# Kernel optimization log

Hardware: AMD Instinct MI355X
Metric: run time of the kernel (lower is better)

The kernel has to match this reference:

```python
import jax, jax.numpy as jnp
import numpy as np

N = 50000
E = 600000
D_IN = 128
D_HID = 128


def gcn_conv(x, src, dst, ew, W, b):
    """PyG-style GCNConv with self-loops and symmetric normalization.
    x: [N, Fin], src/dst: [E'], ew: [E'], W: [Fin, Fout], b: [Fout].
    """
    n = x.shape[0]
    # degree from incoming edge weights (self-loops already appended)
    deg = jax.ops.segment_sum(ew, dst, num_segments=n)
    dinv = jnp.where(deg > 0, jax.lax.rsqrt(deg), 0.0)
    norm = dinv[src] * ew * dinv[dst]  # [E']
    h = x @ W  # linear transform first (PyG order)
    msg = h[src] * norm[:, None]  # gather + scale, [E', Fout]
    out = jax.ops.segment_sum(msg, dst, num_segments=n)  # scatter-add
    return out + b


def setup_inputs() -> dict:
    key = jax.random.key(0)
    k1, k2, k3, k4, k5, k6, k7 = jax.random.split(key, 7)
    x = jax.random.normal(k1, (N, D_IN), dtype=jnp.float32)
    edge_index = jax.random.randint(k2, (2, E), 0, N, dtype=jnp.int64)
    edge_weight = jax.random.uniform(k3, (E,), dtype=jnp.float32)
    s1 = 1.0 / np.sqrt(D_IN)
    s2 = 1.0 / np.sqrt(D_HID)
    W1 = jax.random.uniform(k4, (D_IN, D_HID), dtype=jnp.float32, minval=-s1, maxval=s1)
    b1 = jax.random.uniform(k5, (D_HID,), dtype=jnp.float32, minval=-s1, maxval=s1)
    W2 = jax.random.uniform(k6, (D_HID, D_IN), dtype=jnp.float32, minval=-s2, maxval=s2)
    b2 = jax.random.uniform(k7, (D_IN,), dtype=jnp.float32, minval=-s2, maxval=s2)
    return {"x": x, "edge_index": edge_index, "edge_weight": edge_weight,
            "W1": W1, "b1": b1, "W2": W2, "b2": b2}


def reference(x, edge_index, edge_weight, W1, b1, W2, b2):
    n = x.shape[0]
    loops = jnp.arange(n, dtype=edge_index.dtype)
    src = jnp.concatenate([edge_index[0], loops])
    dst = jnp.concatenate([edge_index[1], loops])
    ew = jnp.concatenate([edge_weight, jnp.ones((n,), dtype=edge_weight.dtype)])
    h = gcn_conv(x, src, dst, ew, W1, b1)
    h = jax.nn.relu(h)
    h = gcn_conv(h, src, dst, ew, W2, b2)
    return jax.nn.sigmoid(h)
```

## Files before the change

### kernel.cpp

```cpp
#include <hip/hip_runtime.h>
#include <math.h>


typedef unsigned int uint32;
typedef unsigned long long u64;
typedef __attribute__((ext_vector_type(8))) short bf16x8;
typedef __attribute__((ext_vector_type(4))) float f32x4;

__device__ __forceinline__ unsigned short f2bf(float f) {
    uint32 b = __float_as_uint(f);
    return (unsigned short)((b + 0x7FFFu + ((b >> 16) & 1u)) >> 16);
}

__device__ __forceinline__ float2 bf2_decode(uint32 u) {
    return make_float2(__uint_as_float(u << 16),
                       __uint_as_float(u & 0xFFFF0000u));
}

__global__ __launch_bounds__(256) void k_hist(const int* __restrict__ dst,
                                              const float* __restrict__ ew,
                                              u64* __restrict__ packed,
                                              int* __restrict__ rank, int e, int nNodes,
                                              const float* __restrict__ W1,
                                              const float* __restrict__ W2,
                                              unsigned short* __restrict__ WT1,
                                              unsigned short* __restrict__ WT2,
                                              int nbE) {
    const int b = blockIdx.x;
    if (b >= nbE) {
        int j = (b - nbE) * 256 + threadIdx.x;
        int k = j >> 7, nn = j & 127;
        WT1[nn * 128 + k] = f2bf(W1[k * 128 + nn]);
        WT2[nn * 128 + k] = f2bf(W2[k * 128 + nn]);
        return;
    }
    int i = b * 256 + threadIdx.x;
    if (i < e) {
        int d = dst[i];
        int r = b & 7;
        u64 add = (1ULL << 44) + (u64)(ew[i] * 4294967296.0f);
        u64 old = atomicAdd(&packed[(size_t)r * nNodes + d], add);
        rank[i] = (int)(old >> 44);
    }
}

__global__ __launch_bounds__(256) void k_scan1(const u64* __restrict__ packed,
                                               float* __restrict__ dinv,
                                               u64* __restrict__ bases,
                                               int* __restrict__ out,
                                               int* __restrict__ sums, int nNodes) {
    __shared__ int s[256];
    const int t = threadIdx.x;
    const int base = blockIdx.x * 1024 + t * 4;
    const int n = nNodes + 1;
    int v[4];
    #pragma unroll
    for (int u = 0; u < 4; ++u) {
        int idx = base + u;
        int c = 0;
        if (idx < nNodes) {
            const u64 mask = (1ULL << 44) - 1;
            u64 ssum = 0;
            u64 bs = 0;
            uint32 cum = 0;
            #pragma unroll
            for (int r = 0; r < 8; ++r) {
                u64 pv = packed[(size_t)r * nNodes + idx];
                bs |= (u64)cum << (8 * r);
                cum += (uint32)(pv >> 44);
                ssum += (pv & mask);
            }
            c = (int)cum;
            float deg = 1.0f + (float)ssum * (1.0f / 4294967296.0f);
            dinv[idx] = rsqrtf(deg);
            bases[idx] = bs;
        }
        v[u] = c;
    }
    s[t] = v[0] + v[1] + v[2] + v[3];
    __syncthreads();
    #pragma unroll
    for (int off = 1; off < 256; off <<= 1) {
        int x = (t >= off) ? s[t - off] : 0;
        __syncthreads();
        s[t] += x;
        __syncthreads();
    }
    if (t == 255) sums[blockIdx.x] = s[255];
    int e = (t == 0) ? 0 : s[t - 1];
    if (base + 0 < n) out[base + 0] = e;
    if (base + 1 < n) out[base + 1] = e + v[0];
    if (base + 2 < n) out[base + 2] = e + v[0] + v[1];
    if (base + 3 < n) out[base + 3] = e + v[0] + v[1] + v[2];
}

__global__ __launch_bounds__(256) void k_scan2(int* __restrict__ sums, int g) {
    __shared__ int s[256];
    const int t = threadIdx.x;
    s[t] = (t < g) ? sums[t] : 0;
    __syncthreads();
    #pragma unroll
    for (int off = 1; off < 256; off <<= 1) {
        int x = (t >= off) ? s[t - off] : 0;
        __syncthreads();
        s[t] += x;
        __syncthreads();
    }
    if (t < g) sums[t] = (t == 0) ? 0 : s[t - 1];
}

__global__ __launch_bounds__(256) void k_fill(const int* __restrict__ src,
                                              const int* __restrict__ dst,
                                              const float* __restrict__ ew,
                                              const float* __restrict__ dinv,
                                              const int* __restrict__ rowptr,
                                              const int* __restrict__ csums,
                                              const u64* __restrict__ bases,
                                              const int* __restrict__ rank,
                                              float2* __restrict__ csr, int e) {
    int i = blockIdx.x * 256 + threadIdx.x;
    if (i < e) {
        int s = src[i], d = dst[i];
        int r = blockIdx.x & 7;
        float nrm = dinv[s] * ew[i] * dinv[d];
        int pos = rowptr[d] + csums[d >> 10]
                + (int)((bases[d] >> (8 * r)) & 0xFF) + rank[i];
        csr[pos] = make_float2(__int_as_float(s), nrm);
    }
}

template <int AFP32>
__global__ __launch_bounds__(256) void k_gemm(const void* __restrict__ Ap,
                                              const unsigned short* __restrict__ WT,
                                              unsigned short* __restrict__ H, int n) {
    const int lane = threadIdx.x & 63;
    const int wv   = threadIdx.x >> 6;
    const int quad = lane >> 4;
    const int l16  = lane & 15;
    const int m0   = blockIdx.x * 128 + wv * 32;
    f32x4 acc[2][8] = {};

    #pragma unroll
    for (int ks = 0; ks < 4; ++ks) {
        const int k0 = ks * 32 + quad * 8;
        bf16x8 a[2];
        #pragma unroll
        for (int rt = 0; rt < 2; ++rt) {
            int row = m0 + rt * 16 + l16;
            if (row >= n) row = n - 1;
            if (AFP32) {
                const float* Af = (const float*)Ap + (size_t)row * 128 + k0;
                float4 f0 = *(const float4*)(Af);
                float4 f1 = *(const float4*)(Af + 4);
                bf16x8 v;
                v[0] = (short)f2bf(f0.x); v[1] = (short)f2bf(f0.y);
                v[2] = (short)f2bf(f0.z); v[3] = (short)f2bf(f0.w);
                v[4] = (short)f2bf(f1.x); v[5] = (short)f2bf(f1.y);
                v[6] = (short)f2bf(f1.z); v[7] = (short)f2bf(f1.w);
                a[rt] = v;
            } else {
                const unsigned short* Ab = (const unsigned short*)Ap + (size_t)row * 128 + k0;
                a[rt] = *(const bf16x8*)Ab;
            }
        }
        #pragma unroll
        for (int ct = 0; ct < 8; ++ct) {
            bf16x8 b = *(const bf16x8*)(WT + (size_t)(ct * 16 + l16) * 128 + k0);
            acc[0][ct] = __builtin_amdgcn_mfma_f32_16x16x32_bf16(a[0], b, acc[0][ct], 0, 0, 0);
            acc[1][ct] = __builtin_amdgcn_mfma_f32_16x16x32_bf16(a[1], b, acc[1][ct], 0, 0, 0);
        }
    }

    #pragma unroll
    for (int rt = 0; rt < 2; ++rt) {
        #pragma unroll
        for (int r = 0; r < 4; ++r) {
            int row = m0 + rt * 16 + quad * 4 + r;
            if (row < n) {
                unsigned short* o = H + (size_t)row * 128 + l16;
                #pragma unroll
                for (int ct = 0; ct < 8; ++ct)
                    o[ct * 16] = f2bf(acc[rt][ct][r]);
            }
        }
    }
}

__device__ __forceinline__ void fma8(float* acc, uint4 u, float w) {
    float2 f;
    f = bf2_decode(u.x); acc[0] += f.x * w; acc[1] += f.y * w;
    f = bf2_decode(u.y); acc[2] += f.x * w; acc[3] += f.y * w;
    f = bf2_decode(u.z); acc[4] += f.x * w; acc[5] += f.y * w;
    f = bf2_decode(u.w); acc[6] += f.x * w; acc[7] += f.y * w;
}

template <int ACT>
__global__ __launch_bounds__(256) void k_gather(const uint4* __restrict__ Hb4,
                                                const float2* __restrict__ csr,
                                                const int* __restrict__ rowptr,
                                                const int* __restrict__ csums,
                                                const float* __restrict__ dinv,
                                                const float4* __restrict__ bias4,
                                                void* __restrict__ outp, int N) {
    int node = blockIdx.x * 4 + (threadIdx.x >> 6);
    if (node >= N) return;
    const int lane = threadIdx.x & 63;
    const int q = lane >> 4, l = lane & 15;
    const int start = rowptr[node] + csums[node >> 10];
    const int end   = rowptr[node + 1] + csums[(node + 1) >> 10];

    float di = dinv[node];
    float selfw = (q == 0) ? di * di : 0.0f;
    float acc[8] = {};
    fma8(acc, Hb4[(size_t)node * 16 + l], selfw);

    for (int k = start; k < end; k += 16) {
        float2 c[4];
        float w[4];
        uint4 u[4];
        #pragma unroll
        for (int j = 0; j < 4; ++j) {
            int ej = k + q + 4 * j;
            c[j] = csr[ej < end ? ej : end - 1];
            w[j] = (ej < end) ? c[j].y : 0.0f;
        }
        #pragma unroll
        for (int j = 0; j < 4; ++j)
            u[j] = Hb4[(size_t)__float_as_int(c[j].x) * 16 + l];
        #pragma unroll
        for (int j = 0; j < 4; ++j)
            fma8(acc, u[j], w[j]);
    }

    #pragma unroll
    for (int j = 0; j < 8; ++j) {
        acc[j] += __shfl_xor(acc[j], 16, 64);
        acc[j] += __shfl_xor(acc[j], 32, 64);
    }

    if (q == 0) {
        float4 b0 = bias4[l * 2], b1 = bias4[l * 2 + 1];
        acc[0] += b0.x; acc[1] += b0.y; acc[2] += b0.z; acc[3] += b0.w;
        acc[4] += b1.x; acc[5] += b1.y; acc[6] += b1.z; acc[7] += b1.w;
        if (ACT == 0) {
            #pragma unroll
            for (int j = 0; j < 8; ++j) acc[j] = fmaxf(acc[j], 0.0f);
            uint4 o;
            o.x = (uint32)f2bf(acc[0]) | ((uint32)f2bf(acc[1]) << 16);
            o.y = (uint32)f2bf(acc[2]) | ((uint32)f2bf(acc[3]) << 16);
            o.z = (uint32)f2bf(acc[4]) | ((uint32)f2bf(acc[5]) << 16);
            o.w = (uint32)f2bf(acc[6]) | ((uint32)f2bf(acc[7]) << 16);
            ((uint4*)outp)[(size_t)node * 16 + l] = o;
        } else {
            #pragma unroll
            for (int j = 0; j < 8; ++j) acc[j] = 1.0f / (1.0f + expf(-acc[j]));
            float4* o4 = (float4*)outp + (size_t)node * 32 + l * 2;
            o4[0] = make_float4(acc[0], acc[1], acc[2], acc[3]);
            o4[1] = make_float4(acc[4], acc[5], acc[6], acc[7]);
        }
    }
}

extern "C" void kernel_launch(void* const* d_in, const int* in_sizes, int n_in,
                              void* d_out, int out_size, void* d_ws, size_t ws_size,
                              hipStream_t stream) {
    const float* x  = (const float*)d_in[0];
    const int*   ei = (const int*)d_in[1];
    const float* ew = (const float*)d_in[2];
    const float* W1 = (const float*)d_in[3];
    const float* b1 = (const float*)d_in[4];
    const float* W2 = (const float*)d_in[5];
    const float* b2 = (const float*)d_in[6];

    const int N = in_sizes[0] / 128;
    const int E = in_sizes[2];
    const int* src = ei;
    const int* dst = ei + E;
    float* out = (float*)d_out;

    auto align = [](size_t v) { return (v + 255) & ~(size_t)255; };
    char* p = (char*)d_ws;
    float*  dinv   = (float*)p;   p += align((size_t)N * 4);
    int*    rowptr = (int*)p;     p += align((size_t)(N + 1) * 4);
    int*    csums  = (int*)p;     p += align((size_t)1024 * 4);
    u64*    bases  = (u64*)p;     p += align((size_t)N * 8);
    unsigned short* WT1 = (unsigned short*)p; p += align((size_t)128 * 128 * 2);
    unsigned short* WT2 = (unsigned short*)p; p += align((size_t)128 * 128 * 2);
    int*    rank   = (int*)p;     p += align((size_t)E * 4);
    float2* csr    = (float2*)p;  p += align((size_t)E * 8);
    unsigned short* h  = (unsigned short*)p; p += align((size_t)N * 128 * 2);
    unsigned short* g1 = (unsigned short*)p;
    u64* packed = (u64*)g1;

    const int nbE = (E + 255) / 256;
    const int gScan = (N + 1 + 1023) / 1024;
    const int gGemm = (N + 127) / 128;
    const int gGath = (N + 3) / 4;

    hipMemsetAsync(packed, 0, (size_t)8 * N * 8, stream);
    k_hist<<<nbE + 64, 256, 0, stream>>>(dst, ew, packed, rank, E, N,
                                         W1, W2, WT1, WT2, nbE);
    k_scan1<<<gScan, 256, 0, stream>>>(packed, dinv, bases, rowptr, csums, N);
    k_scan2<<<1, 256, 0, stream>>>(csums, gScan);
    k_fill<<<nbE, 256, 0, stream>>>(src, dst, ew, dinv, rowptr, csums, bases,
                                    rank, csr, E);

    k_gemm<1><<<gGemm, 256, 0, stream>>>(x, WT1, h, N);
    k_gather<0><<<gGath, 256, 0, stream>>>((const uint4*)h, csr, rowptr, csums,
                                           dinv, (const float4*)b1, g1, N);

    k_gemm<0><<<gGemm, 256, 0, stream>>>(g1, WT2, h, N);
    k_gather<1><<<gGath, 256, 0, stream>>>((const uint4*)h, csr, rowptr, csums,
                                           dinv, (const float4*)b2, out, N);
}
```

Before: 227.8 us.

## Fuse memset/transpose init, merge first GEMM with histogram, single-pass scan

Replaces the memset and histogram launch with an init kernel that zeroes the packed counters and transposes the weights. The first GEMM is merged into the histogram launch so MFMA blocks and atomic blocks share one grid. The two scan kernels become one, with a last-block-done atomic counter doing the block-sum scan. This removes several launches and lets independent work overlap, at the cost of acquire/release atomics and a mixed-work grid that may balance poorly.

```diff
diff --git a/kernel.cpp b/kernel.cpp
--- a/kernel.cpp
+++ b/kernel.cpp
@@ -17,39 +17,112 @@
                        __uint_as_float(u & 0xFFFF0000u));
 }
 
-__global__ __launch_bounds__(256) void k_hist(const int* __restrict__ dst,
-                                              const float* __restrict__ ew,
-                                              u64* __restrict__ packed,
-                                              int* __restrict__ rank, int e, int nNodes,
+template <int AFP32>
+__device__ __forceinline__ void gemm_body(const void* __restrict__ Ap,
+                                          const unsigned short* __restrict__ WT,
+                                          unsigned short* __restrict__ H,
+                                          int n, int tb) {
+    const int lane = threadIdx.x & 63;
+    const int wv   = threadIdx.x >> 6;
+    const int quad = lane >> 4;
+    const int l16  = lane & 15;
+    const int m0   = tb * 128 + wv * 32;
+    f32x4 acc[2][8] = {};
+
+    #pragma unroll
+    for (int ks = 0; ks < 4; ++ks) {
+        const int k0 = ks * 32 + quad * 8;
+        bf16x8 a[2];
+        #pragma unroll
+        for (int rt = 0; rt < 2; ++rt) {
+            int row = m0 + rt * 16 + l16;
+            if (row >= n) row = n - 1;
+            if (AFP32) {
+                const float* Af = (const float*)Ap + (size_t)row * 128 + k0;
+                float4 f0 = *(const float4*)(Af);
+                float4 f1 = *(const float4*)(Af + 4);
+                bf16x8 v;
+                v[0] = (short)f2bf(f0.x); v[1] = (short)f2bf(f0.y);
+                v[2] = (short)f2bf(f0.z); v[3] = (short)f2bf(f0.w);
+                v[4] = (short)f2bf(f1.x); v[5] = (short)f2bf(f1.y);
+                v[6] = (short)f2bf(f1.z); v[7] = (short)f2bf(f1.w);
+                a[rt] = v;
+            } else {
+                const unsigned short* Ab = (const unsigned short*)Ap + (size_t)row * 128 + k0;
+                a[rt] = *(const bf16x8*)Ab;
+            }
+        }
+        #pragma unroll
+        for (int ct = 0; ct < 8; ++ct) {
+            bf16x8 b = *(const bf16x8*)(WT + (size_t)(ct * 16 + l16) * 128 + k0);
+            acc[0][ct] = __builtin_amdgcn_mfma_f32_16x16x32_bf16(a[0], b, acc[0][ct], 0, 0, 0);
+            acc[1][ct] = __builtin_amdgcn_mfma_f32_16x16x32_bf16(a[1], b, acc[1][ct], 0, 0, 0);
+        }
+    }
+
+    #pragma unroll
+    for (int rt = 0; rt < 2; ++rt) {
+        #pragma unroll
+        for (int r = 0; r < 4; ++r) {
+            int row = m0 + rt * 16 + quad * 4 + r;
+            if (row < n) {
+                unsigned short* o = H + (size_t)row * 128 + l16;
+                #pragma unroll
+                for (int ct = 0; ct < 8; ++ct)
+                    o[ct * 16] = f2bf(acc[rt][ct][r]);
+            }
+        }
+    }
+}
+
+__global__ __launch_bounds__(256) void k_init(u64* __restrict__ packed, int n4,
+                                              int* __restrict__ done,
                                               const float* __restrict__ W1,
                                               const float* __restrict__ W2,
                                               unsigned short* __restrict__ WT1,
-                                              unsigned short* __restrict__ WT2,
-                                              int nbE) {
-    const int b = blockIdx.x;
-    if (b >= nbE) {
-        int j = (b - nbE) * 256 + threadIdx.x;
+                                              unsigned short* __restrict__ WT2) {
+    int idx = blockIdx.x * 256 + threadIdx.x;
+    if (idx < n4) ((uint4*)packed)[idx] = make_uint4(0u, 0u, 0u, 0u);
+    if (idx == 0) *done = 0;
+    if (blockIdx.x < 64) {
+        int j = blockIdx.x * 256 + threadIdx.x;
         int k = j >> 7, nn = j & 127;
         WT1[nn * 128 + k] = f2bf(W1[k * 128 + nn]);
         WT2[nn * 128 + k] = f2bf(W2[k * 128 + nn]);
+    }
+}
+
+__global__ __launch_bounds__(256) void k_gemm1_hist(const float* __restrict__ x,
+                                                    const unsigned short* __restrict__ WT1,
+                                                    unsigned short* __restrict__ h,
+                                                    const int* __restrict__ dst,
+                                                    const float* __restrict__ ew,
+                                                    u64* __restrict__ packed,
+                                                    int* __restrict__ rank,
+                                                    int E, int N, int gGemm) {
+    const int b = blockIdx.x;
+    if (b < gGemm) {
+        gemm_body<1>(x, WT1, h, N, b);
         return;
     }
-    int i = b * 256 + threadIdx.x;
-    if (i < e) {
+    int i = (b - gGemm) * 256 + threadIdx.x;
+    if (i < E) {
         int d = dst[i];
-        int r = b & 7;
+        int r = (i >> 8) & 7;
         u64 add = (1ULL << 44) + (u64)(ew[i] * 4294967296.0f);
-        u64 old = atomicAdd(&packed[(size_t)r * nNodes + d], add);
+        u64 old = atomicAdd(&packed[(size_t)r * N + d], add);
         rank[i] = (int)(old >> 44);
     }
 }
 
-__global__ __launch_bounds__(256) void k_scan1(const u64* __restrict__ packed,
-                                               float* __restrict__ dinv,
-                                               u64* __restrict__ bases,
-                                               int* __restrict__ out,
-                                               int* __restrict__ sums, int nNodes) {
+__global__ __launch_bounds__(256) void k_scan(const u64* __restrict__ packed,
+                                              float* __restrict__ dinv,
+                                              u64* __restrict__ bases,
+                                              int* __restrict__ rowptr,
+                                              int* __restrict__ csums,
+                                              int* __restrict__ done, int nNodes) {
     __shared__ int s[256];
+    __shared__ int lastFlag;
     const int t = threadIdx.x;
     const int base = blockIdx.x * 1024 + t * 4;
     const int n = nNodes + 1;
@@ -86,27 +159,35 @@
         s[t] += x;
         __syncthreads();
     }
-    if (t == 255) sums[blockIdx.x] = s[255];
+    if (t == 255)
+        __hip_atomic_store(&csums[blockIdx.x], s[255], __ATOMIC_RELEASE,
+                           __HIP_MEMORY_SCOPE_AGENT);
     int e = (t == 0) ? 0 : s[t - 1];
-    if (base + 0 < n) out[base + 0] = e;
-    if (base + 1 < n) out[base + 1] = e + v[0];
-    if (base + 2 < n) out[base + 2] = e + v[0] + v[1];
-    if (base + 3 < n) out[base + 3] = e + v[0] + v[1] + v[2];
-}
-
-__global__ __launch_bounds__(256) void k_scan2(int* __restrict__ sums, int g) {
-    __shared__ int s[256];
-    const int t = threadIdx.x;
-    s[t] = (t < g) ? sums[t] : 0;
+    if (base + 0 < n) rowptr[base + 0] = e;
+    if (base + 1 < n) rowptr[base + 1] = e + v[0];
+    if (base + 2 < n) rowptr[base + 2] = e + v[0] + v[1];
+    if (base + 3 < n) rowptr[base + 3] = e + v[0] + v[1] + v[2];
+
     __syncthreads();
-    #pragma unroll
-    for (int off = 1; off < 256; off <<= 1) {
-        int x = (t >= off) ? s[t - off] : 0;
-        __syncthreads();
-        s[t] += x;
-        __syncthreads();
-    }
-    if (t < g) sums[t] = (t == 0) ? 0 : s[t - 1];
+    if (t == 0) {
+        int prev = __hip_atomic_fetch_add(done, 1, __ATOMIC_ACQ_REL,
+                                          __HIP_MEMORY_SCOPE_AGENT);
+        lastFlag = (prev == (int)gridDim.x - 1);
+    }
+    __syncthreads();
+    if (lastFlag && t < 64) {
+        int g = (int)gridDim.x;
+        int orig = (t < g) ? __hip_atomic_load(&csums[t], __ATOMIC_ACQUIRE,
+                                               __HIP_MEMORY_SCOPE_AGENT)
+                           : 0;
+        int vv = orig;
+        #pragma unroll
+        for (int off = 1; off < 64; off <<= 1) {
+            int y = __shfl_up(vv, off, 64);
+            if (t >= off) vv += y;
+        }
+        if (t < g) csums[t] = vv - orig;
+    }
 }
 
 __global__ __launch_bounds__(256) void k_fill(const int* __restrict__ src,
@@ -121,7 +202,7 @@
     int i = blockIdx.x * 256 + threadIdx.x;
     if (i < e) {
         int s = src[i], d = dst[i];
-        int r = blockIdx.x & 7;
+        int r = (i >> 8) & 7;
         float nrm = dinv[s] * ew[i] * dinv[d];
         int pos = rowptr[d] + csums[d >> 10]
                 + (int)((bases[d] >> (8 * r)) & 0xFF) + rank[i];
@@ -133,57 +214,7 @@
 __global__ __launch_bounds__(256) void k_gemm(const void* __restrict__ Ap,
                                               const unsigned short* __restrict__ WT,
                                               unsigned short* __restrict__ H, int n) {
-    const int lane = threadIdx.x & 63;
-    const int wv   = threadIdx.x >> 6;
-    const int quad = lane >> 4;
-    const int l16  = lane & 15;
-    const int m0   = blockIdx.x * 128 + wv * 32;
-    f32x4 acc[2][8] = {};
-
-    #pragma unroll
-    for (int ks = 0; ks < 4; ++ks) {
-        const int k0 = ks * 32 + quad * 8;
-        bf16x8 a[2];
-        #pragma unroll
-        for (int rt = 0; rt < 2; ++rt) {
-            int row = m0 + rt * 16 + l16;
-            if (row >= n) row = n - 1;
-            if (AFP32) {
-                const float* Af = (const float*)Ap + (size_t)row * 128 + k0;
-                float4 f0 = *(const float4*)(Af);
-                float4 f1 = *(const float4*)(Af + 4);
-                bf16x8 v;
-                v[0] = (short)f2bf(f0.x); v[1] = (short)f2bf(f0.y);
-                v[2] = (short)f2bf(f0.z); v[3] = (short)f2bf(f0.w);
-                v[4] = (short)f2bf(f1.x); v[5] = (short)f2bf(f1.y);
-                v[6] = (short)f2bf(f1.z); v[7] = (short)f2bf(f1.w);
-                a[rt] = v;
-            } else {
-                const unsigned short* Ab = (const unsigned short*)Ap + (size_t)row * 128 + k0;
-                a[rt] = *(const bf16x8*)Ab;
-            }
-        }
-        #pragma unroll
-        for (int ct = 0; ct < 8; ++ct) {
-            bf16x8 b = *(const bf16x8*)(WT + (size_t)(ct * 16 + l16) * 128 + k0);
-            acc[0][ct] = __builtin_amdgcn_mfma_f32_16x16x32_bf16(a[0], b, acc[0][ct], 0, 0, 0);
-            acc[1][ct] = __builtin_amdgcn_mfma_f32_16x16x32_bf16(a[1], b, acc[1][ct], 0, 0, 0);
-        }
-    }
-
-    #pragma unroll
-    for (int rt = 0; rt < 2; ++rt) {
-        #pragma unroll
-        for (int r = 0; r < 4; ++r) {
-            int row = m0 + rt * 16 + quad * 4 + r;
-            if (row < n) {
-                unsigned short* o = H + (size_t)row * 128 + l16;
-                #pragma unroll
-                for (int ct = 0; ct < 8; ++ct)
-                    o[ct * 16] = f2bf(acc[rt][ct][r]);
-            }
-        }
-    }
+    gemm_body<AFP32>(Ap, WT, H, n, blockIdx.x);
 }
 
 __device__ __forceinline__ void fma8(float* acc, uint4 u, float w) {
@@ -283,6 +314,7 @@
     float*  dinv   = (float*)p;   p += align((size_t)N * 4);
     int*    rowptr = (int*)p;     p += align((size_t)(N + 1) * 4);
     int*    csums  = (int*)p;     p += align((size_t)1024 * 4);
+    int*    done   = (int*)p;     p += align((size_t)256);
     u64*    bases  = (u64*)p;     p += align((size_t)N * 8);
     unsigned short* WT1 = (unsigned short*)p; p += align((size_t)128 * 128 * 2);
     unsigned short* WT2 = (unsigned short*)p; p += align((size_t)128 * 128 * 2);
@@ -296,16 +328,16 @@
     const int gScan = (N + 1 + 1023) / 1024;
     const int gGemm = (N + 127) / 128;
     const int gGath = (N + 3) / 4;
-
-    hipMemsetAsync(packed, 0, (size_t)8 * N * 8, stream);
-    k_hist<<<nbE + 64, 256, 0, stream>>>(dst, ew, packed, rank, E, N,
-                                         W1, W2, WT1, WT2, nbE);
-    k_scan1<<<gScan, 256, 0, stream>>>(packed, dinv, bases, rowptr, csums, N);
-    k_scan2<<<1, 256, 0, stream>>>(csums, gScan);
+    const int n4 = N * 4;
+    const int gInit = ((n4 + 255) / 256) < 64 ? 64 : ((n4 + 255) / 256);
+
+    k_init<<<gInit, 256, 0, stream>>>(packed, n4, done, W1, W2, WT1, WT2);
+    k_gemm1_hist<<<gGemm + nbE, 256, 0, stream>>>(x, WT1, h, dst, ew, packed,
+                                                  rank, E, N, gGemm);
+    k_scan<<<gScan, 256, 0, stream>>>(packed, dinv, bases, rowptr, csums, done, N);
     k_fill<<<nbE, 256, 0, stream>>>(src, dst, ew, dinv, rowptr, csums, bases,
                                     rank, csr, E);
 
-    k_gemm<1><<<gGemm, 256, 0, stream>>>(x, WT1, h, N);
     k_gather<0><<<gGath, 256, 0, stream>>>((const uint4*)h, csr, rowptr, csums,
                                            dinv, (const float4*)b1, g1, N);
 
```

Result: faster. 218.9 us (-3.9%).
